# Kernel optimization log

Hardware: AMD Instinct MI355X
Metric: run time of the kernel (lower is better)

The kernel has to match this reference:

```python
import jax, jax.numpy as jnp
import numpy as np

N_S = 50000
N_T = 50000
D_IN = 256
D_OUT = 128
E = 1600000


def setup_inputs() -> dict:
    key = jax.random.key(0)
    ks = jax.random.split(key, 7)
    inp_s = jax.random.normal(ks[0], (N_S, D_IN), dtype=jnp.float32)
    inp_t = jax.random.normal(ks[1], (N_T, D_IN), dtype=jnp.float32)
    adj_s_idx = jax.random.randint(ks[2], (E, 2), 0, N_S, dtype=jnp.int32)
    adj_s_val = jax.random.uniform(ks[3], (E,), dtype=jnp.float32)
    adj_t_idx = jax.random.randint(ks[4], (E, 2), 0, N_T, dtype=jnp.int32)
    adj_t_val = jax.random.uniform(ks[5], (E,), dtype=jnp.float32)
    # Glorot-uniform shared weights, as in weight_variable_glorot
    init_range = np.sqrt(6.0 / (D_IN + D_OUT))
    W = jax.random.uniform(ks[6], (D_IN, D_OUT), minval=-init_range,
                           maxval=init_range, dtype=jnp.float32)
    return {"inp_s": inp_s, "inp_t": inp_t,
            "adj_s_idx": adj_s_idx, "adj_s_val": adj_s_val,
            "adj_t_idx": adj_t_idx, "adj_t_val": adj_t_val,
            "W": W}


def _spmm(idx, val, x, n_rows):
    # sparse [n_rows, n_cols] @ dense x: gather source rows, scale, scatter-add to dest
    rows, cols = idx[:, 0], idx[:, 1]
    msgs = x[cols] * val[:, None]                      # [E, D_OUT]
    return jax.ops.segment_sum(msgs, rows, num_segments=n_rows)


def _gcn_branch(x, idx, val, W, n_rows):
    # dropout = 0.0 -> identity; dense GEMM -> SpMM -> relu
    h = x @ W                                          # [N, D_OUT]
    h = _spmm(idx, val, h, n_rows)
    return jax.nn.relu(h)


def reference(inp_s, inp_t, adj_s_idx, adj_s_val, adj_t_idx, adj_t_val, W):
    out_s = _gcn_branch(inp_s, adj_s_idx, adj_s_val, W, N_S)
    out_t = _gcn_branch(inp_t, adj_t_idx, adj_t_val, W, N_T)
    return (out_s, out_t)
```

## Files before the change

kernel.cpp:

```cpp
#include <hip/hip_runtime.h>
#include <cstdint>
#include <cstddef>

#define D_IN   256
#define D_OUT  128
#define NB_MAX 256

typedef short bf16x8 __attribute__((ext_vector_type(8)));
typedef float f32x4  __attribute__((ext_vector_type(4)));

union Frag { bf16x8 v; uint32_t u[4]; };

struct Branch {
  const float* X;
  const int*   idx;
  const float* val;
  uint16_t* H;
  int*   ptr;
  int*   bucketTotal;
  int*   bucketBase;
  int*   bucketCur;
  uint64_t* kv2;
  uint32_t* csr4;
  float* out;
};

__device__ inline uint32_t cvt_pk_bf16(float lo, float hi) {
  uint32_t r;
  asm("v_cvt_pk_bf16_f32 %0, %1, %2" : "=v"(r) : "v"(lo), "v"(hi));
  return r;
}

__device__ inline int block_scan256_excl(int v, int tid) {
  int lane = tid & 63, w = tid >> 6;
  int s = v;
  #pragma unroll
  for (int off = 1; off < 64; off <<= 1) {
    int t = __shfl_up(s, off);
    if (lane >= off) s += t;
  }
  __shared__ int wsum[4];
  if (lane == 63) wsum[w] = s;
  __syncthreads();
  int add = 0;
  #pragma unroll
  for (int i = 0; i < 4; ++i) add += (i < w) ? wsum[i] : 0;
  return s + add - v;
}

__global__ __launch_bounds__(256) void wprep3_kernel(const float* __restrict__ W,
                                                     uint16_t* __restrict__ WT3) {
  int n = blockIdx.x;
  int t = threadIdx.x;
  int ks = t >> 5, g = (t >> 3) & 3, j = t & 7;
  int k = ks * 32 + ((j < 4) ? (4 * g + j) : (16 + 4 * g + (j - 4)));
  uint32_t u = __float_as_uint(W[k * 128 + n]);
  WT3[(size_t)((ks * 4 + g) * 128 + n) * 8 + j] =
      (uint16_t)((u + 0x7FFFu + ((u >> 16) & 1u)) >> 16);
}

__global__ __launch_bounds__(256, 3) void gemm_mfma_kernel(const uint16_t* __restrict__ WT3,
                                                           Branch b0, Branch b1, int n_rows) {
  Branch b = blockIdx.y ? b1 : b0;
  const int t = threadIdx.x;
  const int w = t >> 6, l = t & 63;
  const int c = l & 15, g = l >> 4;
  const int row0 = blockIdx.x * 128;

  __shared__ uint8_t sX[2][16384];

  auto stage = [&](int ks, int buf) {
    #pragma unroll
    for (int i = 0; i < 4; ++i) {
      int row = i * 32 + (t >> 3);
      int gr = row0 + row; if (gr > n_rows - 1) gr = n_rows - 1;
      int kb = ((t & 7) * 16) ^ ((row & 7) << 4);
      const float* src = b.X + (size_t)gr * D_IN + ks * 32 + (kb >> 2);
      __builtin_amdgcn_global_load_lds(
          (const __attribute__((address_space(1))) uint32_t*)src,
          (__attribute__((address_space(3))) uint32_t*)&sX[buf][i * 4096 + t * 16],
          16, 0, 0);
    }
  };

  const uint4* Bp = (const uint4*)WT3;

  f32x4 acc[2][8];
  #pragma unroll
  for (int i = 0; i < 2; ++i)
    #pragma unroll
    for (int j = 0; j < 8; ++j) acc[i][j] = (f32x4){0.f, 0.f, 0.f, 0.f};

  stage(0, 0);
  asm volatile("s_waitcnt vmcnt(0)" ::: "memory");
  __syncthreads();

  for (int ks = 0; ks < 8; ++ks) {
    int buf = ks & 1;
    uint4 bu[8];
    #pragma unroll
    for (int nf = 0; nf < 8; ++nf)
      bu[nf] = Bp[(ks * 4 + g) * 128 + nf * 16 + c];
    if (ks < 7) stage(ks + 1, buf ^ 1);

    Frag A[2];
    #pragma unroll
    for (int rf = 0; rf < 2; ++rf) {
      int row = w * 32 + rf * 16 + c;
      const uint8_t* base = &sX[buf][row * 128];
      int swz = (row & 7) << 4;
      float4 x0 = *(const float4*)(base + ((g * 16) ^ swz));
      float4 x1 = *(const float4*)(base + ((64 + g * 16) ^ swz));
      A[rf].u[0] = cvt_pk_bf16(x0.x, x0.y);
      A[rf].u[1] = cvt_pk_bf16(x0.z, x0.w);
      A[rf].u[2] = cvt_pk_bf16(x1.x, x1.y);
      A[rf].u[3] = cvt_pk_bf16(x1.z, x1.w);
    }

    #pragma unroll
    for (int nf = 0; nf < 8; ++nf) {
      Frag B;
      B.u[0] = bu[nf].x; B.u[1] = bu[nf].y; B.u[2] = bu[nf].z; B.u[3] = bu[nf].w;
      acc[0][nf] = __builtin_amdgcn_mfma_f32_16x16x32_bf16(A[0].v, B.v, acc[0][nf], 0, 0, 0);
      acc[1][nf] = __builtin_amdgcn_mfma_f32_16x16x32_bf16(A[1].v, B.v, acc[1][nf], 0, 0, 0);
    }

    if (ks < 7) {
      asm volatile("s_waitcnt vmcnt(0)" ::: "memory");
      __syncthreads();
    }
  }

  #pragma unroll
  for (int rf = 0; rf < 2; ++rf)
    #pragma unroll
    for (int nf = 0; nf < 8; ++nf)
      #pragma unroll
      for (int r = 0; r < 4; ++r) {
        float v = acc[rf][nf][r];
        float o = __shfl_xor(v, 1);
        uint32_t pk = cvt_pk_bf16(v, o);
        uint32_t pk2 = __shfl_xor(pk, 2);
        int row_g = row0 + w * 32 + rf * 16 + 4 * g + r;
        if ((c & 3) == 0 && row_g < n_rows) {
          uint2 d; d.x = pk; d.y = pk2;
          *(uint2*)(b.H + (size_t)row_g * D_OUT + nf * 16 + c) = d;
        }
      }
}

__global__ __launch_bounds__(256) void bucket_count_kernel(Branch b0, Branch b1, int ne, int nb) {
  Branch b = blockIdx.y ? b1 : b0;
  __shared__ int hist[NB_MAX];
  const int tid = threadIdx.x;
  const int base = blockIdx.x * 4096;
  if (tid < nb) hist[tid] = 0;
  __syncthreads();
  #pragma unroll
  for (int i = 0; i < 16; ++i) {
    int e = base + i * 256 + tid;
    if (e < ne) {
      int r = ((const int2*)b.idx)[e].x;
      atomicAdd(&hist[r >> 8], 1);
    }
  }
  __syncthreads();
  if (tid < nb) {
    int h = hist[tid];
    if (h) atomicAdd(&b.bucketTotal[tid], h);
  }
}

__global__ __launch_bounds__(256) void bucket_scan_kernel(Branch b0, Branch b1, int nb, int n, int ne) {
  Branch b = blockIdx.y ? b1 : b0;
  const int tid = threadIdx.x;
  int v = (tid < nb) ? b.bucketTotal[tid] : 0;
  int excl = block_scan256_excl(v, tid);
  if (tid <= nb) b.bucketBase[tid] = excl;
  if (tid < nb)  b.bucketCur[tid]  = excl;
  if (tid == 0)  b.ptr[n] = ne;
}

__global__ __launch_bounds__(256) void bin_kernel(Branch b0, Branch b1, int ne, int nb) {
  Branch b = blockIdx.y ? b1 : b0;
  __shared__ int hist[NB_MAX];
  __shared__ int lcur[NB_MAX];
  __shared__ int gbase[NB_MAX];
  const int tid = threadIdx.x;
  const int base = blockIdx.x * 4096;
  if (tid < nb) hist[tid] = 0;
  __syncthreads();
  uint64_t kv2[16];
  int bkt[16];
  #pragma unroll
  for (int i = 0; i < 16; ++i) {
    int e = base + i * 256 + tid;
    bkt[i] = -1;
    if (e < ne) {
      int2 rc = ((const int2*)b.idx)[e];
      uint32_t v = __float_as_uint(b.val[e]);
      kv2[i] = ((uint64_t)v << 32) | ((uint32_t)rc.x << 16) | (uint32_t)rc.y;
      bkt[i] = rc.x >> 8;
      atomicAdd(&hist[bkt[i]], 1);
    }
  }
  __syncthreads();
  if (tid < nb) {
    int h = hist[tid];
    gbase[tid] = h ? atomicAdd(&b.bucketCur[tid], h) : 0;
    lcur[tid] = 0;
  }
  __syncthreads();
  #pragma unroll
  for (int i = 0; i < 16; ++i) {
    if (bkt[i] >= 0) {
      int dst = gbase[bkt[i]] + atomicAdd(&lcur[bkt[i]], 1);
      b.kv2[dst] = kv2[i];
    }
  }
}

__global__ __launch_bounds__(256) void bucket_csr_kernel(Branch b0, Branch b1, int n) {
  Branch b = blockIdx.y ? b1 : b0;
  const int bkt = blockIdx.x;
  const int tid = threadIdx.x;
  const int beg = b.bucketBase[bkt], end = b.bucketBase[bkt + 1];
  __shared__ int hist[256];
  __shared__ int cur[256];
  hist[tid] = 0;
  __syncthreads();
  for (int e = beg + tid; e < end; e += 256)
    atomicAdd(&hist[(int)((b.kv2[e] >> 16) & 0xFF)], 1);
  __syncthreads();
  int v = hist[tid];
  int excl = block_scan256_excl(v, tid);
  cur[tid] = beg + excl;
  int row = bkt * 256 + tid;
  if (row < n) b.ptr[row] = beg + excl;
  __syncthreads();
  for (int e = beg + tid; e < end; e += 256) {
    uint64_t kv2 = b.kv2[e];
    int r = (int)((kv2 >> 16) & 0xFF);
    uint32_t u = (uint32_t)(kv2 >> 32);
    uint32_t vbf = (u + 0x7FFFu + ((u >> 16) & 1u)) & 0xFFFF0000u;
    int pos = atomicAdd(&cur[r], 1);
    b.csr4[pos] = vbf | (uint32_t)(kv2 & 0xFFFFu);
  }
}

__global__ __launch_bounds__(256) void gather_kernel(Branch b0, Branch b1, int n_rows) {
  const int bid = blockIdx.x;
  const int br  = (bid & 7) >> 2;
  const int local = (bid >> 3) * 4 + (bid & 3);
  Branch b = br ? b1 : b0;
  int row = local * 8 + (threadIdx.x >> 5);
  if (row >= n_rows) return;
  int lane2 = (threadIdx.x & 31) * 2;
  const uint32_t* H32 = (const uint32_t*)b.H;
  int beg = b.ptr[row], end = b.ptr[row + 1];
  float4 acc = make_float4(0.f, 0.f, 0.f, 0.f);

  auto fma_edge = [&](uint32_t e4) {
    int c = (int)(e4 & 0xFFFFu);
    float v = __uint_as_float(e4 & 0xFFFF0000u);
    uint2 h = *(const uint2*)(H32 + (size_t)c * 64 + lane2);
    float h0 = __uint_as_float(h.x << 16);
    float h1 = __uint_as_float(h.x & 0xFFFF0000u);
    float h2 = __uint_as_float(h.y << 16);
    float h3 = __uint_as_float(h.y & 0xFFFF0000u);
    acc.x = fmaf(h0, v, acc.x); acc.y = fmaf(h1, v, acc.y);
    acc.z = fmaf(h2, v, acc.z); acc.w = fmaf(h3, v, acc.w);
  };

  int e = beg;
  for (; e + 8 <= end; e += 8) {
    uint32_t k0 = b.csr4[e + 0], k1 = b.csr4[e + 1];
    uint32_t k2 = b.csr4[e + 2], k3 = b.csr4[e + 3];
    uint32_t k4 = b.csr4[e + 4], k5 = b.csr4[e + 5];
    uint32_t k6 = b.csr4[e + 6], k7 = b.csr4[e + 7];
    fma_edge(k0); fma_edge(k1); fma_edge(k2); fma_edge(k3);
    fma_edge(k4); fma_edge(k5); fma_edge(k6); fma_edge(k7);
  }
  for (; e < end; ++e) fma_edge(b.csr4[e]);

  float4 o;
  o.x = fmaxf(acc.x, 0.f); o.y = fmaxf(acc.y, 0.f);
  o.z = fmaxf(acc.z, 0.f); o.w = fmaxf(acc.w, 0.f);
  *(float4*)&b.out[(size_t)row * D_OUT + (threadIdx.x & 31) * 4] = o;
}

extern "C" void kernel_launch(void* const* d_in, const int* in_sizes, int n_in,
                              void* d_out, int out_size, void* d_ws, size_t ws_size,
                              hipStream_t stream) {
  const float* inp_s = (const float*)d_in[0];
  const float* inp_t = (const float*)d_in[1];
  const int*   idx_s = (const int*)d_in[2];
  const float* val_s = (const float*)d_in[3];
  const int*   idx_t = (const int*)d_in[4];
  const float* val_t = (const float*)d_in[5];
  const float* W     = (const float*)d_in[6];
  float* out = (float*)d_out;

  const int n  = in_sizes[0] / D_IN;
  const int ne = in_sizes[3];
  const int nb = (n + 255) >> 8;

  char* p = (char*)d_ws;
  auto alloc = [&](size_t bytes) -> char* {
    char* r = p;
    p += (bytes + 255) & ~(size_t)255;
    return r;
  };
  uint16_t* H_s    = (uint16_t*)alloc((size_t)n * D_OUT * 2);
  uint16_t* H_t    = (uint16_t*)alloc((size_t)n * D_OUT * 2);
  uint16_t* WT3    = (uint16_t*)alloc((size_t)128 * 256 * 2);
  int* ptr_s       = (int*)alloc((size_t)(n + 1) * 4);
  int* ptr_t       = (int*)alloc((size_t)(n + 1) * 4);
  int* btotal      = (int*)alloc((size_t)2 * NB_MAX * 4);
  int* btotal_s    = btotal;
  int* btotal_t    = btotal + NB_MAX;
  int* bbase_s     = (int*)alloc((size_t)(NB_MAX + 1) * 4);
  int* bbase_t     = (int*)alloc((size_t)(NB_MAX + 1) * 4);
  int* bcur_s      = (int*)alloc(NB_MAX * 4);
  int* bcur_t      = (int*)alloc(NB_MAX * 4);
  uint64_t* kv2_s  = (uint64_t*)alloc((size_t)ne * 8);
  uint64_t* kv2_t  = (uint64_t*)alloc((size_t)ne * 8);
  uint32_t* c4_s   = (uint32_t*)alloc((size_t)ne * 4);
  uint32_t* c4_t   = (uint32_t*)alloc((size_t)ne * 4);

  Branch bs = { inp_s, idx_s, val_s, H_s, ptr_s, btotal_s, bbase_s, bcur_s, kv2_s, c4_s, out };
  Branch bt = { inp_t, idx_t, val_t, H_t, ptr_t, btotal_t, bbase_t, bcur_t, kv2_t, c4_t,
                out + (size_t)n * D_OUT };

  const int nblkE = (ne + 4095) / 4096;
  const int bpb   = (((n + 7) / 8) + 3) & ~3;

  hipMemsetAsync(btotal, 0, (size_t)2 * NB_MAX * 4, stream);
  wprep3_kernel<<<dim3(128), 256, 0, stream>>>(W, WT3);
  gemm_mfma_kernel<<<dim3((n + 127) / 128, 2), 256, 0, stream>>>(WT3, bs, bt, n);
  bucket_count_kernel<<<dim3(nblkE, 2), 256, 0, stream>>>(bs, bt, ne, nb);
  bucket_scan_kernel<<<dim3(1, 2), 256, 0, stream>>>(bs, bt, nb, n, ne);
  bin_kernel<<<dim3(nblkE, 2), 256, 0, stream>>>(bs, bt, ne, nb);
  bucket_csr_kernel<<<dim3(nb, 2), 256, 0, stream>>>(bs, bt, n);
  gather_kernel<<<dim3(2 * bpb), 256, 0, stream>>>(bs, bt, n);
}
```

Before: 214.2 us.

## Fuse bucket counting into GEMM launch and load A operands directly to registers

The bucket histogram kernel is merged into the GEMM launch as a separate z-slice, so the edge counting runs concurrently with the dense GEMM and one launch is removed. The GEMM also drops LDS double-buffering: each wave loads its full 32x256 fp32 A tile straight into registers, converts it to bf16 fragments, then streams W fragments per MFMA. This removes the LDS staging and the barriers, but raises register pressure (occupancy bound lowered to 2) and loses the coalesced async LDS loads.

```diff
diff --git a/kernel.cpp b/kernel.cpp
--- a/kernel.cpp
+++ b/kernel.cpp
@@ -59,75 +59,86 @@
       (uint16_t)((u + 0x7FFFu + ((u >> 16) & 1u)) >> 16);
 }
 
-__global__ __launch_bounds__(256, 3) void gemm_mfma_kernel(const uint16_t* __restrict__ WT3,
-                                                           Branch b0, Branch b1, int n_rows) {
+__global__ __launch_bounds__(256, 2) void gemm_count_kernel(const uint16_t* __restrict__ WT3,
+                                                            Branch b0, Branch b1,
+                                                            int n_rows, int ne, int nb) {
   Branch b = blockIdx.y ? b1 : b0;
   const int t = threadIdx.x;
+  __shared__ int hist[NB_MAX];
+
+  if (blockIdx.z == 1) {
+    const int base = blockIdx.x * 4096;
+    if (t < nb) hist[t] = 0;
+    __syncthreads();
+    #pragma unroll
+    for (int i = 0; i < 16; ++i) {
+      int e = base + i * 256 + t;
+      if (e < ne) {
+        int r = ((const int2*)b.idx)[e].x;
+        atomicAdd(&hist[r >> 8], 1);
+      }
+    }
+    __syncthreads();
+    if (t < nb) {
+      int h = hist[t];
+      if (h) atomicAdd(&b.bucketTotal[t], h);
+    }
+    return;
+  }
+
   const int w = t >> 6, l = t & 63;
   const int c = l & 15, g = l >> 4;
-  const int row0 = blockIdx.x * 128;
-
-  __shared__ uint8_t sX[2][16384];
-
-  auto stage = [&](int ks, int buf) {
-    #pragma unroll
-    for (int i = 0; i < 4; ++i) {
-      int row = i * 32 + (t >> 3);
-      int gr = row0 + row; if (gr > n_rows - 1) gr = n_rows - 1;
-      int kb = ((t & 7) * 16) ^ ((row & 7) << 4);
-      const float* src = b.X + (size_t)gr * D_IN + ks * 32 + (kb >> 2);
-      __builtin_amdgcn_global_load_lds(
-          (const __attribute__((address_space(1))) uint32_t*)src,
-          (__attribute__((address_space(3))) uint32_t*)&sX[buf][i * 4096 + t * 16],
-          16, 0, 0);
-    }
-  };
+  const int row0 = blockIdx.x * 128 + w * 32;
+  if (row0 >= n_rows) return;
+
+  int r0 = row0 + c;      if (r0 > n_rows - 1) r0 = n_rows - 1;
+  int r1 = row0 + 16 + c; if (r1 > n_rows - 1) r1 = n_rows - 1;
+  const float4* X0 = (const float4*)(b.X + (size_t)r0 * D_IN);
+  const float4* X1 = (const float4*)(b.X + (size_t)r1 * D_IN);
+
+  float4 a0[16], a1[16];
+  #pragma unroll
+  for (int i = 0; i < 8; ++i) {
+    a0[2 * i]     = X0[i * 8 + g];
+    a0[2 * i + 1] = X0[i * 8 + 4 + g];
+    a1[2 * i]     = X1[i * 8 + g];
+    a1[2 * i + 1] = X1[i * 8 + 4 + g];
+  }
+  #pragma unroll
+  for (int i = 0; i < 16; ++i) {
+    asm volatile("" :: "v"(a0[i].x), "v"(a0[i].y), "v"(a0[i].z), "v"(a0[i].w));
+    asm volatile("" :: "v"(a1[i].x), "v"(a1[i].y), "v"(a1[i].z), "v"(a1[i].w));
+  }
+
+  Frag A0[8], A1[8];
+  #pragma unroll
+  for (int ks = 0; ks < 8; ++ks) {
+    A0[ks].u[0] = cvt_pk_bf16(a0[2 * ks].x, a0[2 * ks].y);
+    A0[ks].u[1] = cvt_pk_bf16(a0[2 * ks].z, a0[2 * ks].w);
+    A0[ks].u[2] = cvt_pk_bf16(a0[2 * ks + 1].x, a0[2 * ks + 1].y);
+    A0[ks].u[3] = cvt_pk_bf16(a0[2 * ks + 1].z, a0[2 * ks + 1].w);
+    A1[ks].u[0] = cvt_pk_bf16(a1[2 * ks].x, a1[2 * ks].y);
+    A1[ks].u[1] = cvt_pk_bf16(a1[2 * ks].z, a1[2 * ks].w);
+    A1[ks].u[2] = cvt_pk_bf16(a1[2 * ks + 1].x, a1[2 * ks + 1].y);
+    A1[ks].u[3] = cvt_pk_bf16(a1[2 * ks + 1].z, a1[2 * ks + 1].w);
+  }
 
   const uint4* Bp = (const uint4*)WT3;
-
   f32x4 acc[2][8];
   #pragma unroll
   for (int i = 0; i < 2; ++i)
     #pragma unroll
     for (int j = 0; j < 8; ++j) acc[i][j] = (f32x4){0.f, 0.f, 0.f, 0.f};
 
-  stage(0, 0);
-  asm volatile("s_waitcnt vmcnt(0)" ::: "memory");
-  __syncthreads();
-
+  #pragma unroll
   for (int ks = 0; ks < 8; ++ks) {
-    int buf = ks & 1;
-    uint4 bu[8];
-    #pragma unroll
-    for (int nf = 0; nf < 8; ++nf)
-      bu[nf] = Bp[(ks * 4 + g) * 128 + nf * 16 + c];
-    if (ks < 7) stage(ks + 1, buf ^ 1);
-
-    Frag A[2];
-    #pragma unroll
-    for (int rf = 0; rf < 2; ++rf) {
-      int row = w * 32 + rf * 16 + c;
-      const uint8_t* base = &sX[buf][row * 128];
-      int swz = (row & 7) << 4;
-      float4 x0 = *(const float4*)(base + ((g * 16) ^ swz));
-      float4 x1 = *(const float4*)(base + ((64 + g * 16) ^ swz));
-      A[rf].u[0] = cvt_pk_bf16(x0.x, x0.y);
-      A[rf].u[1] = cvt_pk_bf16(x0.z, x0.w);
-      A[rf].u[2] = cvt_pk_bf16(x1.x, x1.y);
-      A[rf].u[3] = cvt_pk_bf16(x1.z, x1.w);
-    }
-
     #pragma unroll
     for (int nf = 0; nf < 8; ++nf) {
+      uint4 bu = Bp[(ks * 4 + g) * 128 + nf * 16 + c];
       Frag B;
-      B.u[0] = bu[nf].x; B.u[1] = bu[nf].y; B.u[2] = bu[nf].z; B.u[3] = bu[nf].w;
-      acc[0][nf] = __builtin_amdgcn_mfma_f32_16x16x32_bf16(A[0].v, B.v, acc[0][nf], 0, 0, 0);
-      acc[1][nf] = __builtin_amdgcn_mfma_f32_16x16x32_bf16(A[1].v, B.v, acc[1][nf], 0, 0, 0);
-    }
-
-    if (ks < 7) {
-      asm volatile("s_waitcnt vmcnt(0)" ::: "memory");
-      __syncthreads();
+      B.u[0] = bu.x; B.u[1] = bu.y; B.u[2] = bu.z; B.u[3] = bu.w;
+      acc[0][nf] = __builtin_amdgcn_mfma_f32_16x16x32_bf16(A0[ks].v, B.v, acc[0][nf], 0, 0, 0);
+      acc[1][nf] = __builtin_amdgcn_mfma_f32_16x16x32_bf16(A1[ks].v, B.v, acc[1][nf], 0, 0, 0);
     }
   }
 
@@ -141,34 +152,12 @@
         float o = __shfl_xor(v, 1);
         uint32_t pk = cvt_pk_bf16(v, o);
         uint32_t pk2 = __shfl_xor(pk, 2);
-        int row_g = row0 + w * 32 + rf * 16 + 4 * g + r;
+        int row_g = row0 + rf * 16 + 4 * g + r;
         if ((c & 3) == 0 && row_g < n_rows) {
           uint2 d; d.x = pk; d.y = pk2;
           *(uint2*)(b.H + (size_t)row_g * D_OUT + nf * 16 + c) = d;
         }
       }
-}
-
-__global__ __launch_bounds__(256) void bucket_count_kernel(Branch b0, Branch b1, int ne, int nb) {
-  Branch b = blockIdx.y ? b1 : b0;
-  __shared__ int hist[NB_MAX];
-  const int tid = threadIdx.x;
-  const int base = blockIdx.x * 4096;
-  if (tid < nb) hist[tid] = 0;
-  __syncthreads();
-  #pragma unroll
-  for (int i = 0; i < 16; ++i) {
-    int e = base + i * 256 + tid;
-    if (e < ne) {
-      int r = ((const int2*)b.idx)[e].x;
-      atomicAdd(&hist[r >> 8], 1);
-    }
-  }
-  __syncthreads();
-  if (tid < nb) {
-    int h = hist[tid];
-    if (h) atomicAdd(&b.bucketTotal[tid], h);
-  }
 }
 
 __global__ __launch_bounds__(256) void bucket_scan_kernel(Branch b0, Branch b1, int nb, int n, int ne) {
@@ -333,12 +322,13 @@
                 out + (size_t)n * D_OUT };
 
   const int nblkE = (ne + 4095) / 4096;
+  const int nblkG = (n + 127) / 128;
+  const int nblkF = nblkE > nblkG ? nblkE : nblkG;
   const int bpb   = (((n + 7) / 8) + 3) & ~3;
 
   hipMemsetAsync(btotal, 0, (size_t)2 * NB_MAX * 4, stream);
   wprep3_kernel<<<dim3(128), 256, 0, stream>>>(W, WT3);
-  gemm_mfma_kernel<<<dim3((n + 127) / 128, 2), 256, 0, stream>>>(WT3, bs, bt, n);
-  bucket_count_kernel<<<dim3(nblkE, 2), 256, 0, stream>>>(bs, bt, ne, nb);
+  gemm_count_kernel<<<dim3(nblkF, 2, 2), 256, 0, stream>>>(WT3, bs, bt, n, ne, nb);
   bucket_scan_kernel<<<dim3(1, 2), 256, 0, stream>>>(bs, bt, nb, n, ne);
   bin_kernel<<<dim3(nblkE, 2), 256, 0, stream>>>(bs, bt, ne, nb);
   bucket_csr_kernel<<<dim3(nb, 2), 256, 0, stream>>>(bs, bt, n);
```

Result: slower. 229.9 us (+7.3%).

## Merge edge binning and dense GEMM into one launch so they overlap

Applied to the files above, without the earlier changes.

Merges the edge-binning kernel and the MFMA GEMM kernel into a single launch, using blockIdx.z to choose the role and sharing one 32 KB LDS buffer. The GEMM now runs after the bucket count and scan, sharing a grid with binning. The memory-bound scatter can then overlap the compute-heavy GEMM and one launch gap goes away. In exchange, every block reserves the GEMM's LDS and register budget, which may lower occupancy for the binning blocks, and surplus blocks in the padded grid exit early.

```diff
diff --git a/kernel.cpp b/kernel.cpp
--- a/kernel.cpp
+++ b/kernel.cpp
@@ -59,15 +59,88 @@
       (uint16_t)((u + 0x7FFFu + ((u >> 16) & 1u)) >> 16);
 }
 
-__global__ __launch_bounds__(256, 3) void gemm_mfma_kernel(const uint16_t* __restrict__ WT3,
-                                                           Branch b0, Branch b1, int n_rows) {
+__global__ __launch_bounds__(256) void bucket_count_kernel(Branch b0, Branch b1, int ne, int nb) {
+  Branch b = blockIdx.y ? b1 : b0;
+  __shared__ int hist[NB_MAX];
+  const int tid = threadIdx.x;
+  const int base = blockIdx.x * 4096;
+  if (tid < nb) hist[tid] = 0;
+  __syncthreads();
+  #pragma unroll
+  for (int i = 0; i < 16; ++i) {
+    int e = base + i * 256 + tid;
+    if (e < ne) {
+      int r = ((const int2*)b.idx)[e].x;
+      atomicAdd(&hist[r >> 8], 1);
+    }
+  }
+  __syncthreads();
+  if (tid < nb) {
+    int h = hist[tid];
+    if (h) atomicAdd(&b.bucketTotal[tid], h);
+  }
+}
+
+__global__ __launch_bounds__(256) void bucket_scan_kernel(Branch b0, Branch b1, int nb, int n, int ne) {
+  Branch b = blockIdx.y ? b1 : b0;
+  const int tid = threadIdx.x;
+  int v = (tid < nb) ? b.bucketTotal[tid] : 0;
+  int excl = block_scan256_excl(v, tid);
+  if (tid <= nb) b.bucketBase[tid] = excl;
+  if (tid < nb)  b.bucketCur[tid]  = excl;
+  if (tid == 0)  b.ptr[n] = ne;
+}
+
+__global__ __launch_bounds__(256, 3) void bin_gemm_kernel(const uint16_t* __restrict__ WT3,
+                                                          Branch b0, Branch b1,
+                                                          int n_rows, int ne, int nb) {
   Branch b = blockIdx.y ? b1 : b0;
   const int t = threadIdx.x;
+  __shared__ uint8_t smem[32768];
+
+  if (blockIdx.z == 0) {
+    int* hist  = (int*)smem;
+    int* lcur  = hist + NB_MAX;
+    int* gbase = lcur + NB_MAX;
+    const int base = blockIdx.x * 4096;
+    if (base >= ne) return;
+    if (t < nb) hist[t] = 0;
+    __syncthreads();
+    uint64_t kv2[16];
+    int bkt[16];
+    #pragma unroll
+    for (int i = 0; i < 16; ++i) {
+      int e = base + i * 256 + t;
+      bkt[i] = -1;
+      if (e < ne) {
+        int2 rc = ((const int2*)b.idx)[e];
+        uint32_t v = __float_as_uint(b.val[e]);
+        kv2[i] = ((uint64_t)v << 32) | ((uint32_t)rc.x << 16) | (uint32_t)rc.y;
+        bkt[i] = rc.x >> 8;
+        atomicAdd(&hist[bkt[i]], 1);
+      }
+    }
+    __syncthreads();
+    if (t < nb) {
+      int h = hist[t];
+      gbase[t] = h ? atomicAdd(&b.bucketCur[t], h) : 0;
+      lcur[t] = 0;
+    }
+    __syncthreads();
+    #pragma unroll
+    for (int i = 0; i < 16; ++i) {
+      if (bkt[i] >= 0) {
+        int dst = gbase[bkt[i]] + atomicAdd(&lcur[bkt[i]], 1);
+        b.kv2[dst] = kv2[i];
+      }
+    }
+    return;
+  }
+
   const int w = t >> 6, l = t & 63;
   const int c = l & 15, g = l >> 4;
   const int row0 = blockIdx.x * 128;
-
-  __shared__ uint8_t sX[2][16384];
+  if (row0 >= n_rows) return;
 
   auto stage = [&](int ks, int buf) {
     #pragma unroll
@@ -78,7 +151,7 @@
       const float* src = b.X + (size_t)gr * D_IN + ks * 32 + (kb >> 2);
       __builtin_amdgcn_global_load_lds(
           (const __attribute__((address_space(1))) uint32_t*)src,
-          (__attribute__((address_space(3))) uint32_t*)&sX[buf][i * 4096 + t * 16],
+          (__attribute__((address_space(3))) uint32_t*)&smem[buf * 16384 + i * 4096 + t * 16],
           16, 0, 0);
     }
   };
@@ -107,7 +180,7 @@
     #pragma unroll
     for (int rf = 0; rf < 2; ++rf) {
       int row = w * 32 + rf * 16 + c;
-      const uint8_t* base = &sX[buf][row * 128];
+      const uint8_t* base = &smem[buf * 16384 + row * 128];
       int swz = (row & 7) << 4;
       float4 x0 = *(const float4*)(base + ((g * 16) ^ swz));
       float4 x1 = *(const float4*)(base + ((64 + g * 16) ^ swz));
@@ -147,77 +220,6 @@
           *(uint2*)(b.H + (size_t)row_g * D_OUT + nf * 16 + c) = d;
         }
       }
-}
-
-__global__ __launch_bounds__(256) void bucket_count_kernel(Branch b0, Branch b1, int ne, int nb) {
-  Branch b = blockIdx.y ? b1 : b0;
-  __shared__ int hist[NB_MAX];
-  const int tid = threadIdx.x;
-  const int base = blockIdx.x * 4096;
-  if (tid < nb) hist[tid] = 0;
-  __syncthreads();
-  #pragma unroll
-  for (int i = 0; i < 16; ++i) {
-    int e = base + i * 256 + tid;
-    if (e < ne) {
-      int r = ((const int2*)b.idx)[e].x;
-      atomicAdd(&hist[r >> 8], 1);
-    }
-  }
-  __syncthreads();
-  if (tid < nb) {
-    int h = hist[tid];
-    if (h) atomicAdd(&b.bucketTotal[tid], h);
-  }
-}
-
-__global__ __launch_bounds__(256) void bucket_scan_kernel(Branch b0, Branch b1, int nb, int n, int ne) {
-  Branch b = blockIdx.y ? b1 : b0;
-  const int tid = threadIdx.x;
-  int v = (tid < nb) ? b.bucketTotal[tid] : 0;
-  int excl = block_scan256_excl(v, tid);
-  if (tid <= nb) b.bucketBase[tid] = excl;
-  if (tid < nb)  b.bucketCur[tid]  = excl;
-  if (tid == 0)  b.ptr[n] = ne;
-}
-
-__global__ __launch_bounds__(256) void bin_kernel(Branch b0, Branch b1, int ne, int nb) {
-  Branch b = blockIdx.y ? b1 : b0;
-  __shared__ int hist[NB_MAX];
-  __shared__ int lcur[NB_MAX];
-  __shared__ int gbase[NB_MAX];
-  const int tid = threadIdx.x;
-  const int base = blockIdx.x * 4096;
-  if (tid < nb) hist[tid] = 0;
-  __syncthreads();
-  uint64_t kv2[16];
-  int bkt[16];
-  #pragma unroll
-  for (int i = 0; i < 16; ++i) {
-    int e = base + i * 256 + tid;
-    bkt[i] = -1;
-    if (e < ne) {
-      int2 rc = ((const int2*)b.idx)[e];
-      uint32_t v = __float_as_uint(b.val[e]);
-      kv2[i] = ((uint64_t)v << 32) | ((uint32_t)rc.x << 16) | (uint32_t)rc.y;
-      bkt[i] = rc.x >> 8;
-      atomicAdd(&hist[bkt[i]], 1);
-    }
-  }
-  __syncthreads();
-  if (tid < nb) {
-    int h = hist[tid];
-    gbase[tid] = h ? atomicAdd(&b.bucketCur[tid], h) : 0;
-    lcur[tid] = 0;
-  }
-  __syncthreads();
-  #pragma unroll
-  for (int i = 0; i < 16; ++i) {
-    if (bkt[i] >= 0) {
-      int dst = gbase[bkt[i]] + atomicAdd(&lcur[bkt[i]], 1);
-      b.kv2[dst] = kv2[i];
-    }
-  }
 }
 
 __global__ __launch_bounds__(256) void bucket_csr_kernel(Branch b0, Branch b1, int n) {
@@ -333,14 +335,15 @@
                 out + (size_t)n * D_OUT };
 
   const int nblkE = (ne + 4095) / 4096;
+  const int nblkG = (n + 127) / 128;
+  const int nblkF = nblkE > nblkG ? nblkE : nblkG;
   const int bpb   = (((n + 7) / 8) + 3) & ~3;
 
   hipMemsetAsync(btotal, 0, (size_t)2 * NB_MAX * 4, stream);
   wprep3_kernel<<<dim3(128), 256, 0, stream>>>(W, WT3);
-  gemm_mfma_kernel<<<dim3((n + 127) / 128, 2), 256, 0, stream>>>(WT3, bs, bt, n);
   bucket_count_kernel<<<dim3(nblkE, 2), 256, 0, stream>>>(bs, bt, ne, nb);
   bucket_scan_kernel<<<dim3(1, 2), 256, 0, stream>>>(bs, bt, nb, n, ne);
-  bin_kernel<<<dim3(nblkE, 2), 256, 0, stream>>>(bs, bt, ne, nb);
+  bin_gemm_kernel<<<dim3(nblkF, 2, 2), 256, 0, stream>>>(WT3, bs, bt, n, ne, nb);
   bucket_csr_kernel<<<dim3(nb, 2), 256, 0, stream>>>(bs, bt, n);
   gather_kernel<<<dim3(2 * bpb), 256, 0, stream>>>(bs, bt, n);
 }
```

After: 213.8 us. No clear change (-0.2%).
